# Kernel tuning notes

Hardware: AMD Instinct MI355X
Metric: run time of the kernel (lower is better)

Reference implementation:

```python
import jax, jax.numpy as jnp
import numpy as np

HEADS = 16
HIDDEN = 1024
DH = HIDDEN // HEADS
STD = 0.02


def setup_inputs() -> dict:
    key = jax.random.key(0)
    ks = jax.random.split(key, 12)
    B, S = 4, 2048
    inp = {
        'q': jax.random.normal(ks[0], (B, S, HIDDEN), jnp.float32),
        'k': jax.random.normal(ks[1], (B, S, HIDDEN), jnp.float32),
        'v': jax.random.normal(ks[2], (B, S, HIDDEN), jnp.float32),
        'mask': jax.random.randint(ks[3], (B, S), 0, 2, jnp.int32),
        # linear layers: weight [out,in] torch-style, init N(0, 0.02), bias 0
        'wq': STD * jax.random.normal(ks[4], (HIDDEN, HIDDEN), jnp.float32),
        'bq': jnp.zeros((HIDDEN,), jnp.float32),
        'wk': STD * jax.random.normal(ks[5], (HIDDEN, HIDDEN), jnp.float32),
        'bk': jnp.zeros((HIDDEN,), jnp.float32),
        'wv': STD * jax.random.normal(ks[6], (HIDDEN, HIDDEN), jnp.float32),
        'bv': jnp.zeros((HIDDEN,), jnp.float32),
        'wo': STD * jax.random.normal(ks[7], (HIDDEN, HIDDEN), jnp.float32),
        'bo': jnp.zeros((HIDDEN,), jnp.float32),
    }
    return inp


def _split_heads(x):
    B, S, _ = x.shape
    return x.reshape(B, S, HEADS, DH).transpose(0, 2, 1, 3)  # [B,H,S,dh]


def reference(q, k, v, mask, wq, bq, wk, bk, wv, bv, wo, bo):
    B, S, _ = q.shape
    qh = _split_heads(q @ wq.T + bq)
    kh = _split_heads(k @ wk.T + bk)
    vh = _split_heads(v @ wv.T + bv)
    scale = 1.0 / jnp.sqrt(jnp.float32(DH))
    corr = jnp.einsum('bhqd,bhkd->bhqk', qh, kh) * scale  # [B,H,S,S]
    # original masks QUERY rows: mask [B,S] -> [B,1,S,1] broadcast over heads & keys
    row_mask = (mask != 0)[:, None, :, None]
    corr = jnp.where(row_mask, corr, jnp.float32(-1e9))
    prob = jax.nn.softmax(corr, axis=-1)
    # dropout p=0.0 (eval / deterministic reference)
    hidden = jnp.einsum('bhqk,bhkd->bhqd', prob, vh)
    hidden = hidden.transpose(0, 2, 1, 3).reshape(B, S, HIDDEN)
    return hidden @ wo.T + bo
```

## Files before the change

kernel.cpp:

```cpp
#include <hip/hip_runtime.h>

#define BATCH 4
#define SEQ 2048
#define HEADS 16
#define DHEAD 64
#define HID 1024
#define MROWS (BATCH * SEQ)
#define QSCALE 0.1803368801111092f

typedef unsigned short u16;
typedef unsigned int u32;
typedef __attribute__((ext_vector_type(4))) float f32x4;
typedef __attribute__((ext_vector_type(8))) short bf16x8;
typedef __attribute__((ext_vector_type(2))) unsigned int u32x2;
typedef __attribute__((ext_vector_type(4))) unsigned int u32x4;

#define MFMA16(a, b, c) __builtin_amdgcn_mfma_f32_16x16x32_bf16((a), (b), (c), 0, 0, 0)
#define EXP2F(x) __builtin_amdgcn_exp2f(x)

__device__ __forceinline__ u16 f2bf(float f) {
  union { float f; u32 i; } x; x.f = f;
  u32 r = x.i + 0x7fffu + ((x.i >> 16) & 1u);
  return (u16)(r >> 16);
}

__device__ __forceinline__ u32 cvtpk(float a, float b) {
  u32 d;
  asm("v_cvt_pk_bf16_f32 %0, %1, %2" : "=v"(d) : "v"(a), "v"(b));
  return d;
}

__device__ __forceinline__ void lds16(const u16* g, u16* s) {
  __builtin_amdgcn_global_load_lds(
      (const __attribute__((address_space(1))) void*)g,
      (__attribute__((address_space(3))) void*)s, 16, 0, 0);
}

__device__ __forceinline__ void stage8f(const float* __restrict__ g, u16* s) {
  const float4 a = *(const float4*)g;
  const float4 b = *(const float4*)(g + 4);
  ushort4 lo, hi;
  lo.x = f2bf(a.x); lo.y = f2bf(a.y); lo.z = f2bf(a.z); lo.w = f2bf(a.w);
  hi.x = f2bf(b.x); hi.y = f2bf(b.y); hi.z = f2bf(b.z); hi.w = f2bf(b.w);
  *(ushort4*)s = lo;
  *(ushort4*)(s + 4) = hi;
}

struct CvtArgs {
  const float* src[7];
  u16* dst[7];
};
__global__ __launch_bounds__(256) void cvt7(CvtArgs args, int yoff, int nact) {
  const int y = blockIdx.y + yoff;
  const int i = (blockIdx.x * 256 + threadIdx.x) * 8;
  if (y < 3) {
    if (i < nact) stage8f(args.src[y] + i, args.dst[y] + i);
  } else {
    if (i < 4 * (1 << 20)) {
      const int j = i >> 20, off = i & ((1 << 20) - 1);
      stage8f(args.src[3 + j] + off, args.dst[3 + j] + off);
    }
  }
}

template<bool ADMA, bool BDMA>
__device__ __forceinline__ void gemm_core(
    const void* __restrict__ Av, const void* __restrict__ Wv,
    int tid, int m0, int n0, u16* As, u16* Bs, f32x4 (&acc)[4][4])
{
  const int srow = tid >> 2, cslot = tid & 3;
  const int gc = cslot ^ ((srow >> 1) & 3);
  const int w = tid >> 6, l = tid & 63;
  const int quad = l >> 4, l15 = l & 15;
  const int sw = (l15 >> 1) & 3;
  const int wm = (w & 1) << 6, wn = (w >> 1) << 6;

  for (int k0 = 0; k0 < HID; k0 += 32) {
    if (ADMA) {
      const u16* ag = (const u16*)Av + (size_t)(m0 + srow) * HID + k0 + gc * 8;
      lds16(ag, &As[tid * 8]);
      lds16(ag + (size_t)64 * HID, &As[2048 + tid * 8]);
    } else {
      const float* ag = (const float*)Av + (size_t)(m0 + srow) * HID + k0 + gc * 8;
      stage8f(ag, &As[srow * 32 + cslot * 8]);
      stage8f(ag + (size_t)64 * HID, &As[(64 + srow) * 32 + cslot * 8]);
    }
    if (BDMA) {
      const u16* bg = (const u16*)Wv + (size_t)(n0 + srow) * HID + k0 + gc * 8;
      lds16(bg, &Bs[tid * 8]);
      lds16(bg + (size_t)64 * HID, &Bs[2048 + tid * 8]);
    } else {
      const float* bg = (const float*)Wv + (size_t)(n0 + srow) * HID + k0 + gc * 8;
      stage8f(bg, &Bs[srow * 32 + cslot * 8]);
      stage8f(bg + (size_t)64 * HID, &Bs[(64 + srow) * 32 + cslot * 8]);
    }
    __syncthreads();

    bf16x8 a[4], b[4];
    #pragma unroll
    for (int i = 0; i < 4; ++i)
      a[i] = *(const bf16x8*)&As[(wm + i * 16 + l15) * 32 + (quad ^ sw) * 8];
    #pragma unroll
    for (int j = 0; j < 4; ++j)
      b[j] = *(const bf16x8*)&Bs[(wn + j * 16 + l15) * 32 + (quad ^ sw) * 8];
    #pragma unroll
    for (int i = 0; i < 4; ++i)
      #pragma unroll
      for (int j = 0; j < 4; ++j)
        acc[i][j] = MFMA16(a[i], b[j], acc[i][j]);
    __syncthreads();
  }
}

template<bool ADMA, bool BDMA>
__global__ __launch_bounds__(256) void gemm_qkv(
    const void* __restrict__ xq, const void* __restrict__ xk,
    const void* __restrict__ xv,
    const void* __restrict__ wqv, const void* __restrict__ wkv,
    const void* __restrict__ wvv,
    const float* __restrict__ bq, const float* __restrict__ bk,
    const float* __restrict__ bv, const int* __restrict__ Mask,
    u16* __restrict__ qh, u16* __restrict__ kh, u16* __restrict__ vt)
{
  __shared__ u16 As[128 * 32];
  __shared__ u16 Bs[128 * 32];
  const int z = blockIdx.z;
  const void* A = (z == 0) ? xq : (z == 1) ? xk : xv;
  const void* W = (z == 0) ? wqv : (z == 1) ? wkv : wvv;
  const float* Bias = (z == 0) ? bq : (z == 1) ? bk : bv;

  const int tid = threadIdx.x;
  const int m0 = blockIdx.x << 7, n0 = blockIdx.y << 7;
  f32x4 acc[4][4] = {};
  gemm_core<ADMA, BDMA>(A, W, tid, m0, n0, As, Bs, acc);

  const int w = tid >> 6, l = tid & 63;
  const int quad = l >> 4, l15 = l & 15;
  const int wm = (w & 1) << 6, wn = (w >> 1) << 6;

  if (z <= 1) {
    u16* Out = (z == 0) ? qh : kh;
    #pragma unroll
    for (int i = 0; i < 4; ++i) {
      float fl[4];
      #pragma unroll
      for (int r = 0; r < 4; ++r) {
        const int m = m0 + wm + i * 16 + (quad << 2) + r;
        fl[r] = (z == 0) ? (Mask[m] ? QSCALE : 0.f) : 1.f;
      }
      #pragma unroll
      for (int j = 0; j < 4; ++j) {
        const int n = n0 + wn + j * 16 + l15;
        const float bias = Bias[n];
        const int h = n >> 6, d = n & 63;
        #pragma unroll
        for (int r = 0; r < 4; ++r) {
          const int m = m0 + wm + i * 16 + (quad << 2) + r;
          const int bb = m >> 11, s = m & (SEQ - 1);
          Out[((size_t)(bb * HEADS + h) * SEQ + s) * DHEAD + d] =
              f2bf((acc[i][j][r] + bias) * fl[r]);
        }
      }
    }
  } else {
    const int sblk = (m0 + wm) & (SEQ - 1);
    const int bb = (m0 + wm) >> 11;
    #pragma unroll
    for (int j = 0; j < 4; ++j) {
      const int n = n0 + wn + j * 16 + l15;
      const float bias = Bias[n];
      const int h = n >> 6, d = n & 63;
      u16* base = vt + ((size_t)(bb * HEADS + h) * DHEAD + d) * SEQ + sblk;
      #pragma unroll
      for (int r = 0; r < 4; ++r) {
        u32x2 pk;
        pk.x = cvtpk(acc[0][j][r] + bias, acc[1][j][r] + bias);
        pk.y = cvtpk(acc[2][j][r] + bias, acc[3][j][r] + bias);
        *(u32x2*)(base + ((quad << 2) + r) * 4) = pk;
      }
    }
  }
}

template<bool BDMA>
__global__ __launch_bounds__(256) void gemm_out(
    const u16* __restrict__ hidden, const void* __restrict__ wov,
    const float* __restrict__ bo, float* __restrict__ Out)
{
  __shared__ u16 As[128 * 32];
  __shared__ u16 Bs[128 * 32];
  const int tid = threadIdx.x;
  const int m0 = blockIdx.x << 7, n0 = blockIdx.y << 7;
  f32x4 acc[4][4] = {};
  gemm_core<true, BDMA>(hidden, wov, tid, m0, n0, As, Bs, acc);

  const int w = tid >> 6, l = tid & 63;
  const int quad = l >> 4, l15 = l & 15;
  const int wm = (w & 1) << 6, wn = (w >> 1) << 6;
  #pragma unroll
  for (int j = 0; j < 4; ++j) {
    const int n = n0 + wn + j * 16 + l15;
    const float bias = bo[n];
    #pragma unroll
    for (int i = 0; i < 4; ++i) {
      const int mb = m0 + wm + i * 16 + (quad << 2);
      #pragma unroll
      for (int r = 0; r < 4; ++r)
        Out[(size_t)(mb + r) * HID + n] = acc[i][j][r] + bias;
    }
  }
}

__global__ __launch_bounds__(128, 2) void attn_mfma(
    const u16* __restrict__ QH, const u16* __restrict__ KH,
    const u16* __restrict__ VT, u16* __restrict__ Hidden)
{
  __shared__ u16 Qs[2][128 * 32];
  __shared__ u16 Ks[2][2048];
  __shared__ u16 Vt[2][4096];

  const int tid = threadIdx.x;
  const int w = tid >> 6, l = tid & 63;
  const int quad = l >> 4, l15 = l & 15;
  const int sw = (l15 >> 1) & 3;
  const int srow = tid >> 2, cslot = tid & 3;
  const int gc = cslot ^ ((srow >> 1) & 3);
  const int vd = tid >> 3;
  const int vc = (tid & 7) ^ (vd & 7);

  const int lin = blockIdx.y * 16 + blockIdx.x;
  const int bh = lin & 63, b = bh >> 4, h = bh & 15;
  const int q0 = (lin >> 6) << 7;

  const u16* qbase = QH + (size_t)bh * SEQ * DHEAD;
  const u16* kbase = KH + (size_t)bh * SEQ * DHEAD;
  const u16* vbase = VT + (size_t)bh * DHEAD * SEQ;

  #pragma unroll
  for (int hh = 0; hh < 2; ++hh)
    #pragma unroll
    for (int part = 0; part < 4; ++part)
      lds16(qbase + (size_t)(q0 + part * 32 + srow) * DHEAD + hh * 32 + gc * 8,
            &Qs[hh][part * 1024 + tid * 8]);
  #pragma unroll
  for (int hh = 0; hh < 2; ++hh)
    #pragma unroll
    for (int part = 0; part < 2; ++part)
      lds16(kbase + (size_t)(part * 32 + srow) * DHEAD + hh * 32 + gc * 8,
            &Ks[hh][part * 1024 + tid * 8]);
  #pragma unroll
  for (int part = 0; part < 4; ++part)
    lds16(vbase + (size_t)(part * 16 + vd) * SEQ + vc * 8,
          &Vt[0][part * 1024 + tid * 8]);
  asm volatile("s_waitcnt vmcnt(8)" ::: "memory");
  __builtin_amdgcn_s_barrier();

  bf16x8 aq[2][4];
  #pragma unroll
  for (int hh = 0; hh < 2; ++hh)
    #pragma unroll
    for (int j = 0; j < 4; ++j)
      aq[hh][j] = *(const bf16x8*)
          &Qs[hh][(w * 64 + j * 16 + l15) * 32 + (quad ^ sw) * 8];

  const bf16x8 ones8 = {0x3F80, 0x3F80, 0x3F80, 0x3F80,
                        0x3F80, 0x3F80, 0x3F80, 0x3F80};
  f32x4 o[4][4] = {};
  f32x4 lacc[4] = {};
  int cur = 0;

  for (int it = 0; it < SEQ / 64; ++it) {
    asm volatile("s_waitcnt vmcnt(4)" ::: "memory");
    __builtin_amdgcn_s_barrier();

    f32x4 s[4][4] = {};
    __builtin_amdgcn_s_setprio(1);
    #pragma unroll
    for (int i = 0; i < 4; ++i)
      #pragma unroll
      for (int hh = 0; hh < 2; ++hh) {
        const bf16x8 ak = *(const bf16x8*)
            &Ks[hh][(i * 16 + l15) * 32 + (quad ^ sw) * 8];
        #pragma unroll
        for (int j = 0; j < 4; ++j)
          s[i][j] = MFMA16(ak, aq[hh][j], s[i][j]);
      }
    __builtin_amdgcn_s_setprio(0);
    __builtin_amdgcn_s_barrier();

    const int tn = ((it + 1) & (SEQ / 64 - 1)) << 6;
    #pragma unroll
    for (int hh = 0; hh < 2; ++hh)
      #pragma unroll
      for (int part = 0; part < 2; ++part)
        lds16(kbase + (size_t)(tn + part * 32 + srow) * DHEAD + hh * 32 + gc * 8,
              &Ks[hh][part * 1024 + tid * 8]);
    #pragma unroll
    for (int part = 0; part < 4; ++part)
      lds16(vbase + (size_t)(part * 16 + vd) * SEQ + tn + vc * 8,
            &Vt[cur ^ 1][part * 1024 + tid * 8]);

    bf16x8 bp[2][4];
    #pragma unroll
    for (int j = 0; j < 4; ++j) {
      float p[4][4];
      #pragma unroll
      for (int i = 0; i < 4; ++i)
        #pragma unroll
        for (int r = 0; r < 4; ++r)
          p[i][r] = EXP2F(s[i][j][r]);
      u32x4 t0, t1;
      t0.x = cvtpk(p[0][0], p[1][0]); t0.y = cvtpk(p[2][0], p[3][0]);
      t0.z = cvtpk(p[0][1], p[1][1]); t0.w = cvtpk(p[2][1], p[3][1]);
      t1.x = cvtpk(p[0][2], p[1][2]); t1.y = cvtpk(p[2][2], p[3][2]);
      t1.z = cvtpk(p[0][3], p[1][3]); t1.w = cvtpk(p[2][3], p[3][3]);
      bp[0][j] = __builtin_bit_cast(bf16x8, t0);
      bp[1][j] = __builtin_bit_cast(bf16x8, t1);
      lacc[j] = MFMA16(ones8, bp[0][j], lacc[j]);
      lacc[j] = MFMA16(ones8, bp[1][j], lacc[j]);
    }

    asm volatile("s_waitcnt vmcnt(8)" ::: "memory");
    __builtin_amdgcn_s_barrier();

    __builtin_amdgcn_s_setprio(1);
    #pragma unroll
    for (int hh = 0; hh < 2; ++hh)
      #pragma unroll
      for (int m = 0; m < 4; ++m) {
        const int d = m * 16 + l15;
        const bf16x8 av = *(const bf16x8*)
            &Vt[cur][d * 64 + (((quad * 2 + hh) ^ (d & 7)) << 3)];
        #pragma unroll
        for (int j = 0; j < 4; ++j)
          o[m][j] = MFMA16(av, bp[hh][j], o[m][j]);
      }
    __builtin_amdgcn_s_setprio(0);
    cur ^= 1;
  }
  asm volatile("s_waitcnt vmcnt(0)" ::: "memory");

  float inv[4];
  #pragma unroll
  for (int j = 0; j < 4; ++j)
    inv[j] = 1.f / lacc[j][0];

  #pragma unroll
  for (int m = 0; m < 4; ++m)
    #pragma unroll
    for (int j = 0; j < 4; ++j) {
      u32x2 pk;
      pk.x = cvtpk(o[m][j][0] * inv[j], o[m][j][1] * inv[j]);
      pk.y = cvtpk(o[m][j][2] * inv[j], o[m][j][3] * inv[j]);
      *(u32x2*)&Hidden[(size_t)(b * SEQ + q0 + w * 64 + j * 16 + l15) * HID
                       + h * DHEAD + m * 16 + quad * 4] = pk;
    }
}

extern "C" void kernel_launch(void* const* d_in, const int* in_sizes, int n_in,
                              void* d_out, int out_size, void* d_ws, size_t ws_size,
                              hipStream_t stream) {
  const float* q  = (const float*)d_in[0];
  const float* k  = (const float*)d_in[1];
  const float* v  = (const float*)d_in[2];
  const int* mask = (const int*)d_in[3];
  const float* wq = (const float*)d_in[4];
  const float* bq = (const float*)d_in[5];
  const float* wk = (const float*)d_in[6];
  const float* bk = (const float*)d_in[7];
  const float* wv = (const float*)d_in[8];
  const float* bv = (const float*)d_in[9];
  const float* wo = (const float*)d_in[10];
  const float* bo = (const float*)d_in[11];

  const size_t SEG = (size_t)MROWS * HID;
  const size_t WSEG = (size_t)HID * HID;
  const dim3 gq(MROWS / 128, HID / 128, 3);
  const dim3 go(MROWS / 128, HID / 128);
  const dim3 ga(SEQ / 128, BATCH * HEADS);

  const size_t planFULL = (6 * SEG + 4 * WSEG) * sizeof(u16);
  const size_t planMID  = (4 * SEG + 4 * WSEG) * sizeof(u16);

  if (ws_size >= planFULL) {
    u16* qb  = (u16*)d_ws;
    u16* kb  = qb + SEG;
    u16* vb  = kb + SEG;
    u16* qh  = vb + SEG;
    u16* kh  = qh + SEG;
    u16* vt  = kh + SEG;
    u16* wqb = vt + SEG;
    u16* wkb = wqb + WSEG;
    u16* wvb = wkb + WSEG;
    u16* wob = wvb + WSEG;
    u16* hidden = qb;

    CvtArgs ca;
    ca.src[0] = q;  ca.dst[0] = qb;
    ca.src[1] = k;  ca.dst[1] = kb;
    ca.src[2] = v;  ca.dst[2] = vb;
    ca.src[3] = wq; ca.dst[3] = wqb;
    ca.src[4] = wk; ca.dst[4] = wkb;
    ca.src[5] = wv; ca.dst[5] = wvb;
    ca.src[6] = wo; ca.dst[6] = wob;
    cvt7<<<dim3(SEG / 2048, 4), 256, 0, stream>>>(ca, 0, (int)SEG);

    gemm_qkv<true, true><<<gq, 256, 0, stream>>>(qb, kb, vb, wqb, wkb, wvb,
                                                 bq, bk, bv, mask, qh, kh, vt);
    attn_mfma<<<ga, 128, 0, stream>>>(qh, kh, vt, hidden);
    gemm_out<true><<<go, 256, 0, stream>>>(hidden, wob, bo, (float*)d_out);
  } else if (ws_size >= planMID) {
    u16* wqb = (u16*)d_ws;
    u16* wkb = wqb + WSEG;
    u16* wvb = wkb + WSEG;
    u16* wob = wvb + WSEG;
    u16* qh = wob + WSEG;
    u16* kh = qh + SEG;
    u16* vt = kh + SEG;
    u16* hidden = vt + SEG;

    CvtArgs ca;
    ca.src[0] = ca.src[1] = ca.src[2] = q;
    ca.dst[0] = ca.dst[1] = ca.dst[2] = wqb;
    ca.src[3] = wq; ca.dst[3] = wqb;
    ca.src[4] = wk; ca.dst[4] = wkb;
    ca.src[5] = wv; ca.dst[5] = wvb;
    ca.src[6] = wo; ca.dst[6] = wob;
    cvt7<<<dim3(4 * WSEG / 2048, 1), 256, 0, stream>>>(ca, 3, 0);

    gemm_qkv<false, true><<<gq, 256, 0, stream>>>(q, k, v, wqb, wkb, wvb,
                                                  bq, bk, bv, mask, qh, kh, vt);
    attn_mfma<<<ga, 128, 0, stream>>>(qh, kh, vt, hidden);
    gemm_out<true><<<go, 256, 0, stream>>>(hidden, wob, bo, (float*)d_out);
  } else {
    u16* qh = (u16*)d_ws;
    u16* kh = qh + SEG;
    u16* vt = kh + SEG;
    u16* hidden = vt + SEG;

    gemm_qkv<false, false><<<gq, 256, 0, stream>>>(q, k, v, wq, wk, wv,
                                                   bq, bk, bv, mask, qh, kh, vt);
    attn_mfma<<<ga, 128, 0, stream>>>(qh, kh, vt, hidden);
    gemm_out<false><<<go, 256, 0, stream>>>(hidden, wo, bo, (float*)d_out);
  }
}
```

Measured before the change: 328.9 us.

## Use 256x128 tile GEMMs with 512-thread blocks and grid swizzle for projections

Adds new QKV and output projection GEMM kernels built on a shared core that computes 256x128 output tiles with 8 waves, a K-step of 64, XOR-swizzled LDS and double-buffered direct-to-LDS loads. Block indices are remapped so consecutive blocks share rows and columns for better L2 reuse. The larger tiles cut global and LDS traffic per FLOP, but each block now holds more LDS, so only one block fits per CU and the grid has fewer blocks, which may hurt latency hiding and load balance. Only the largest-workspace plan uses the new kernels.

Measured after the change: 322.3 us. -2.0%, faster.

```diff
diff --git a/kernel.cpp b/kernel.cpp
--- a/kernel.cpp
+++ b/kernel.cpp
@@ -211,6 +211,177 @@
   }
 }
 
+__device__ __forceinline__ void core256(
+    const u16* __restrict__ A, const u16* __restrict__ W,
+    int tid, int m0, int n0, u16* As2, u16* Bs2, f32x4 (&acc)[4][4])
+{
+  const int l = tid & 63;
+  const int quad = l >> 4, l15 = l & 15;
+  const int sw7 = l15 & 7;
+  const int w = tid >> 6;
+  const int wm = (w & 3) << 6, wn = (w >> 2) << 6;
+  const int srow = tid >> 3, sslot = tid & 7;
+  const int sgc = sslot ^ (srow & 7);
+
+  const u16* aB = A + (size_t)(m0 + srow) * HID + sgc * 8;
+  const u16* bB = W + (size_t)(n0 + srow) * HID + sgc * 8;
+
+  #pragma unroll
+  for (int p = 0; p < 4; ++p)
+    lds16(aB + (size_t)p * 64 * HID, As2 + p * 4096 + tid * 8);
+  #pragma unroll
+  for (int p = 0; p < 2; ++p)
+    lds16(bB + (size_t)p * 64 * HID, Bs2 + p * 4096 + tid * 8);
+
+  #pragma unroll 2
+  for (int t = 0; t < HID / 64; ++t) {
+    const int c = t & 1;
+    asm volatile("s_waitcnt vmcnt(0)" ::: "memory");
+    __builtin_amdgcn_s_barrier();
+    __builtin_amdgcn_sched_barrier(0);
+
+    if (t < HID / 64 - 1) {
+      const int kk = (t + 1) << 6;
+      u16* ad = As2 + (c ^ 1) * 16384;
+      u16* bd = Bs2 + (c ^ 1) * 8192;
+      #pragma unroll
+      for (int p = 0; p < 4; ++p)
+        lds16(aB + (size_t)p * 64 * HID + kk, ad + p * 4096 + tid * 8);
+      #pragma unroll
+      for (int p = 0; p < 2; ++p)
+        lds16(bB + (size_t)p * 64 * HID + kk, bd + p * 4096 + tid * 8);
+    }
+
+    const u16* Ab = As2 + c * 16384;
+    const u16* Bb = Bs2 + c * 8192;
+    #pragma unroll
+    for (int ks = 0; ks < 2; ++ks) {
+      const int cc = ((ks << 2) | quad) ^ sw7;
+      bf16x8 a[4], b[4];
+      #pragma unroll
+      for (int i = 0; i < 4; ++i)
+        a[i] = *(const bf16x8*)&Ab[(wm + i * 16 + l15) * 64 + cc * 8];
+      #pragma unroll
+      for (int j = 0; j < 4; ++j)
+        b[j] = *(const bf16x8*)&Bb[(wn + j * 16 + l15) * 64 + cc * 8];
+      __builtin_amdgcn_s_setprio(1);
+      #pragma unroll
+      for (int i = 0; i < 4; ++i)
+        #pragma unroll
+        for (int j = 0; j < 4; ++j)
+          acc[i][j] = MFMA16(a[i], b[j], acc[i][j]);
+      __builtin_amdgcn_s_setprio(0);
+    }
+  }
+  asm volatile("s_waitcnt vmcnt(0)" ::: "memory");
+}
+
+__global__ __launch_bounds__(512, 1) void gemm_qkv2(
+    const u16* __restrict__ xq, const u16* __restrict__ xk,
+    const u16* __restrict__ xv,
+    const u16* __restrict__ wqv, const u16* __restrict__ wkv,
+    const u16* __restrict__ wvv,
+    const float* __restrict__ bq, const float* __restrict__ bk,
+    const float* __restrict__ bv, const int* __restrict__ Mask,
+    u16* __restrict__ qh, u16* __restrict__ kh, u16* __restrict__ vt)
+{
+  __shared__ u16 As2[2 * 16384];
+  __shared__ u16 Bs2[2 * 8192];
+  const int tid = threadIdx.x;
+
+  const int lin = blockIdx.x;
+  const int nid = (lin & 7) * 96 + (lin >> 3);
+  const int z = nid >> 8;
+  const int rem = nid & 255;
+  const int m0 = (rem >> 3) << 8, n0 = (rem & 7) << 7;
+
+  const u16* A = (z == 0) ? xq : (z == 1) ? xk : xv;
+  const u16* W = (z == 0) ? wqv : (z == 1) ? wkv : wvv;
+  const float* Bias = (z == 0) ? bq : (z == 1) ? bk : bv;
+
+  f32x4 acc[4][4] = {};
+  core256(A, W, tid, m0, n0, As2, Bs2, acc);
+
+  const int w = tid >> 6, l = tid & 63;
+  const int quad = l >> 4, l15 = l & 15;
+  const int wm = (w & 3) << 6, wn = (w >> 2) << 6;
+
+  if (z <= 1) {
+    u16* Out = (z == 0) ? qh : kh;
+    #pragma unroll
+    for (int i = 0; i < 4; ++i) {
+      float fl[4];
+      #pragma unroll
+      for (int r = 0; r < 4; ++r) {
+        const int m = m0 + wm + i * 16 + (quad << 2) + r;
+        fl[r] = (z == 0) ? (Mask[m] ? QSCALE : 0.f) : 1.f;
+      }
+      #pragma unroll
+      for (int j = 0; j < 4; ++j) {
+        const int n = n0 + wn + j * 16 + l15;
+        const float bias = Bias[n];
+        const int h = n >> 6, d = n & 63;
+        #pragma unroll
+        for (int r = 0; r < 4; ++r) {
+          const int m = m0 + wm + i * 16 + (quad << 2) + r;
+          const int bb = m >> 11, s = m & (SEQ - 1);
+          Out[((size_t)(bb * HEADS + h) * SEQ + s) * DHEAD + d] =
+              f2bf((acc[i][j][r] + bias) * fl[r]);
+        }
+      }
+    }
+  } else {
+    const int sblk = (m0 + wm) & (SEQ - 1);
+    const int bb = (m0 + wm) >> 11;
+    #pragma unroll
+    for (int j = 0; j < 4; ++j) {
+      const int n = n0 + wn + j * 16 + l15;
+      const float bias = Bias[n];
+      const int h = n >> 6, d = n & 63;
+      u16* base = vt + ((size_t)(bb * HEADS + h) * DHEAD + d) * SEQ + sblk;
+      #pragma unroll
+      for (int r = 0; r < 4; ++r) {
+        u32x2 pk;
+        pk.x = cvtpk(acc[0][j][r] + bias, acc[1][j][r] + bias);
+        pk.y = cvtpk(acc[2][j][r] + bias, acc[3][j][r] + bias);
+        *(u32x2*)(base + ((quad << 2) + r) * 4) = pk;
+      }
+    }
+  }
+}
+
+__global__ __launch_bounds__(512, 1) void gemm_out2(
+    const u16* __restrict__ hidden, const u16* __restrict__ wov,
+    const float* __restrict__ bo, float* __restrict__ Out)
+{
+  __shared__ u16 As2[2 * 16384];
+  __shared__ u16 Bs2[2 * 8192];
+  const int tid = threadIdx.x;
+
+  const int lin = blockIdx.x;
+  const int nid = (lin & 7) * 32 + (lin >> 3);
+  const int m0 = (nid >> 3) << 8, n0 = (nid & 7) << 7;
+
+  f32x4 acc[4][4] = {};
+  core256(hidden, wov, tid, m0, n0, As2, Bs2, acc);
+
+  const int w = tid >> 6, l = tid & 63;
+  const int quad = l >> 4, l15 = l & 15;
+  const int wm = (w & 3) << 6, wn = (w >> 2) << 6;
+  #pragma unroll
+  for (int j = 0; j < 4; ++j) {
+    const int n = n0 + wn + j * 16 + l15;
+    const float bias = bo[n];
+    #pragma unroll
+    for (int i = 0; i < 4; ++i) {
+      const int mb = m0 + wm + i * 16 + (quad << 2);
+      #pragma unroll
+      for (int r = 0; r < 4; ++r)
+        Out[(size_t)(mb + r) * HID + n] = acc[i][j][r] + bias;
+    }
+  }
+}
+
 __global__ __launch_bounds__(128, 2) void attn_mfma(
     const u16* __restrict__ QH, const u16* __restrict__ KH,
     const u16* __restrict__ VT, u16* __restrict__ Hidden)
@@ -405,10 +576,10 @@
     ca.src[6] = wo; ca.dst[6] = wob;
     cvt7<<<dim3(SEG / 2048, 4), 256, 0, stream>>>(ca, 0, (int)SEG);
 
-    gemm_qkv<true, true><<<gq, 256, 0, stream>>>(qb, kb, vb, wqb, wkb, wvb,
-                                                 bq, bk, bv, mask, qh, kh, vt);
+    gemm_qkv2<<<dim3(768), 512, 0, stream>>>(qb, kb, vb, wqb, wkb, wvb,
+                                             bq, bk, bv, mask, qh, kh, vt);
     attn_mfma<<<ga, 128, 0, stream>>>(qh, kh, vt, hidden);
-    gemm_out<true><<<go, 256, 0, stream>>>(hidden, wob, bo, (float*)d_out);
+    gemm_out2<<<dim3(256), 512, 0, stream>>>(hidden, wob, bo, (float*)d_out);
   } else if (ws_size >= planMID) {
     u16* wqb = (u16*)d_ws;
     u16* wkb = wqb + WSEG;
```
